# Optimization experiments

Measured on AMD Instinct MI355X. Metric: run time of the kernel, lower is better.

Reference implementation:

```python
import jax, jax.numpy as jnp
import numpy as np

N, E, IN_DIM, HID, HEADS, NUM_GRAPHS = 50000, 400000, 128, 64, 4, 256
WIDTH = HID * HEADS  # 256
NEG_SLOPE = 0.2


def setup_inputs() -> dict:
    key = jax.random.key(0)
    ks = jax.random.split(key, 20)
    inp = {
        'x': jax.random.normal(ks[0], (N, IN_DIM), dtype=jnp.float32),
        'edge_index': jax.random.randint(ks[1], (2, E), 0, N, dtype=jnp.int64),
        'edge_attr': jax.random.normal(ks[2], (E, 4), dtype=jnp.float32),
        'batch': jnp.sort(jax.random.randint(ks[3], (N,), 0, NUM_GRAPHS, dtype=jnp.int64)),
    }
    kidx = 4
    for l, in_ch in enumerate([IN_DIM, WIDTH, WIDTH]):
        s = 1.0 / np.sqrt(in_ch)
        inp[f'W{l}'] = jax.random.normal(ks[kidx], (in_ch, WIDTH), dtype=jnp.float32) * s
        inp[f'a_src{l}'] = jax.random.normal(ks[kidx + 1], (HEADS, HID), dtype=jnp.float32) * 0.1
        inp[f'a_dst{l}'] = jax.random.normal(ks[kidx + 2], (HEADS, HID), dtype=jnp.float32) * 0.1
        inp[f'b{l}'] = jnp.zeros((WIDTH,), dtype=jnp.float32)
        kidx += 3
    inp['lin_w'] = jax.random.normal(ks[kidx], (WIDTH, 1), dtype=jnp.float32) * (1.0 / np.sqrt(WIDTH))
    inp['lin_b'] = jnp.zeros((1,), dtype=jnp.float32)
    return inp


def gat_layer(x, src, dst, W, a_src, a_dst, b):
    n = x.shape[0]
    h = (x @ W).reshape(n, HEADS, HID)                      # [N,H,C]
    al_s = jnp.einsum('nhc,hc->nh', h, a_src)               # [N,H]
    al_d = jnp.einsum('nhc,hc->nh', h, a_dst)
    e = jax.nn.leaky_relu(al_s[src] + al_d[dst], NEG_SLOPE)  # [E,H]
    # segment softmax over destination node (every node has a self-loop)
    m = jax.ops.segment_max(e, dst, num_segments=n)
    e = jnp.exp(e - m[dst])
    denom = jax.ops.segment_sum(e, dst, num_segments=n)
    alpha = e / (denom[dst] + 1e-16)                         # [E,H]
    msg = h[src] * alpha[:, :, None]                         # [E,H,C]
    out = jax.ops.segment_sum(msg, dst, num_segments=n)
    return out.reshape(n, WIDTH) + b


def reference(x, edge_index, edge_attr, batch,
              W0, a_src0, a_dst0, b0,
              W1, a_src1, a_dst1, b1,
              W2, a_src2, a_dst2, b2,
              lin_w, lin_b):
    # PyG GATConv adds self-loops by default
    loops = jnp.arange(N, dtype=edge_index.dtype)
    src = jnp.concatenate([edge_index[0], loops])
    dst = jnp.concatenate([edge_index[1], loops])
    h = x
    for (W, a_s, a_d, b) in [(W0, a_src0, a_dst0, b0),
                             (W1, a_src1, a_dst1, b1),
                             (W2, a_src2, a_dst2, b2)]:
        h = jax.nn.elu(gat_layer(h, src, dst, W, a_s, a_d, b))
    pooled = jax.ops.segment_sum(h, batch, num_segments=NUM_GRAPHS)  # [G,256]
    out = pooled @ lin_w + lin_b                                     # [G,1]
    return out.squeeze(-1)
```

## Files before the change

### kernel.cpp

```cpp
#include <hip/hip_runtime.h>
#include <hip/hip_bf16.h>

#define N_NODES 50000
#define N_EDGES 400000
#define IN_DIM_ 128
#define WIDTH_ 256
#define HEADS_ 4
#define HID_ 64
#define NUM_GRAPHS_ 256
#define NEG_SLOPE_ 0.2f
#define HROW 50048

using s16x8 = __attribute__((ext_vector_type(8))) short;
using f32x4 = __attribute__((ext_vector_type(4))) float;

__device__ inline void split1(float x, short& h, short& l) {
    unsigned int u = __float_as_uint(x);
    h = (short)(u >> 16);
    float hf = __uint_as_float(u & 0xffff0000u);
    float r = x - hf;
    l = (short)(__float_as_uint(r) >> 16);
}
__device__ inline float join1(short h, short l) {
    return __uint_as_float(((unsigned int)(unsigned short)h) << 16) +
           __uint_as_float(((unsigned int)(unsigned short)l) << 16);
}

__global__ void hist_kernel(const int* __restrict__ dst, int* __restrict__ deg) {
    int e = blockIdx.x * blockDim.x + threadIdx.x;
    if (e < N_EDGES) atomicAdd(&deg[dst[e]], 1);
}

__global__ void scan1_kernel(const int* __restrict__ deg, int* __restrict__ rowptr,
                             int* __restrict__ partials) {
    __shared__ int s[256];
    int t = threadIdx.x;
    int gid = blockIdx.x * 256 + t;
    int v = (gid < N_NODES) ? deg[gid] : 0;
    s[t] = v;
    __syncthreads();
    for (int off = 1; off < 256; off <<= 1) {
        int x = 0;
        if (t >= off) x = s[t - off];
        __syncthreads();
        if (t >= off) s[t] += x;
        __syncthreads();
    }
    if (gid < N_NODES) rowptr[gid] = s[t] - v;
    if (t == 255) partials[blockIdx.x] = s[255];
}

__global__ void scan2_kernel(int* __restrict__ partials, int nb) {
    __shared__ int s[256];
    int t = threadIdx.x;
    int v = (t < nb) ? partials[t] : 0;
    s[t] = v;
    __syncthreads();
    for (int off = 1; off < 256; off <<= 1) {
        int x = 0;
        if (t >= off) x = s[t - off];
        __syncthreads();
        if (t >= off) s[t] += x;
        __syncthreads();
    }
    if (t < nb) partials[t] = s[t] - v;
}

__global__ void scan3_kernel(int* __restrict__ rowptr, const int* __restrict__ partials) {
    int gid = blockIdx.x * 256 + threadIdx.x;
    if (gid < N_NODES) rowptr[gid] += partials[blockIdx.x];
    if (gid == 0) rowptr[N_NODES] = N_EDGES;
}

__global__ void scatter_kernel(const int* __restrict__ src, const int* __restrict__ dst,
                               const int* __restrict__ rowptr, int* __restrict__ cursor,
                               int* __restrict__ csr_src) {
    int e = blockIdx.x * blockDim.x + threadIdx.x;
    if (e < N_EDGES) {
        int d = dst[e];
        int pos = rowptr[d] + atomicAdd(&cursor[d], 1);
        csr_src[pos] = src[e];
    }
}

template <int K>
__global__ void split4_kernel(const float* __restrict__ in, short* __restrict__ hi,
                              short* __restrict__ lo) {
    int idx = blockIdx.x * blockDim.x + threadIdx.x;
    if (idx >= HROW * K / 4) return;
    int e0 = idx << 2;
    int row = e0 / K;
    float4 v = make_float4(0.f, 0.f, 0.f, 0.f);
    if (row < N_NODES) v = *(const float4*)&in[e0];
    short4 h, l;
    split1(v.x, h.x, l.x);
    split1(v.y, h.y, l.y);
    split1(v.z, h.z, l.z);
    split1(v.w, h.w, l.w);
    *(short4*)&hi[e0] = h;
    *(short4*)&lo[e0] = l;
}

__global__ void wsplit_kernel(const float* __restrict__ W, short* __restrict__ Whi,
                              short* __restrict__ Wlo, int K) {
    int idx = blockIdx.x * blockDim.x + threadIdx.x;
    if (idx >= K * 256) return;
    int k = idx >> 8, n = idx & 255;
    short h, l;
    split1(W[idx], h, l);
    Whi[n * K + k] = h;
    Wlo[n * K + k] = l;
}

template <int K>
__global__ __launch_bounds__(256) void mfma_gemm(const short* __restrict__ Ahi,
                                                 const short* __restrict__ Alo,
                                                 const short* __restrict__ Bhi,
                                                 const short* __restrict__ Blo,
                                                 float* __restrict__ C) {
    const int tid = threadIdx.x;
    const int lane = tid & 63;
    const int wid = tid >> 6;
    const int wm = wid >> 1, wn = wid & 1;
    const int row0 = blockIdx.x * 128 + wm * 64;
    const int col0 = blockIdx.y * 128 + wn * 64;
    const int lr = lane & 15;
    const int lk = (lane >> 4) << 3;

    f32x4 acc[4][4] = {};

    for (int kk = 0; kk < K; kk += 32) {
        s16x8 ah[4], av[4], bh[4], bv[4];
#pragma unroll
        for (int r = 0; r < 4; ++r) {
            size_t ai = (size_t)(row0 + r * 16 + lr) * K + kk + lk;
            ah[r] = *(const s16x8*)&Ahi[ai];
            av[r] = *(const s16x8*)&Alo[ai];
            size_t bi = (size_t)(col0 + r * 16 + lr) * K + kk + lk;
            bh[r] = *(const s16x8*)&Bhi[bi];
            bv[r] = *(const s16x8*)&Blo[bi];
        }
#pragma unroll
        for (int i = 0; i < 4; ++i)
#pragma unroll
            for (int j = 0; j < 4; ++j) {
                acc[i][j] = __builtin_amdgcn_mfma_f32_16x16x32_bf16(ah[i], bh[j], acc[i][j], 0, 0, 0);
                acc[i][j] = __builtin_amdgcn_mfma_f32_16x16x32_bf16(ah[i], bv[j], acc[i][j], 0, 0, 0);
                acc[i][j] = __builtin_amdgcn_mfma_f32_16x16x32_bf16(av[i], bh[j], acc[i][j], 0, 0, 0);
            }
    }
    const int rb = (lane >> 4) << 2;
#pragma unroll
    for (int i = 0; i < 4; ++i)
#pragma unroll
        for (int q = 0; q < 4; ++q) {
            int r = row0 + i * 16 + rb + q;
#pragma unroll
            for (int j = 0; j < 4; ++j)
                C[(size_t)r * WIDTH_ + col0 + j * 16 + lr] = acc[i][j][q];
        }
}

__global__ void al_kernel(const float* __restrict__ hl, const float* __restrict__ a_src,
                          const float* __restrict__ a_dst, float* __restrict__ als,
                          float* __restrict__ ald) {
    int wid = (blockIdx.x * blockDim.x + threadIdx.x) >> 6;
    int lane = threadIdx.x & 63;
    if (wid >= N_NODES) return;
    const float4 hv = *(const float4*)&hl[(size_t)wid * WIDTH_ + (lane << 2)];
    int hd = lane >> 4;
    int j0 = (lane & 15) << 2;
    const float4 as = *(const float4*)&a_src[hd * HID_ + j0];
    const float4 ad = *(const float4*)&a_dst[hd * HID_ + j0];
    float ps = hv.x * as.x + hv.y * as.y + hv.z * as.z + hv.w * as.w;
    float pd = hv.x * ad.x + hv.y * ad.y + hv.z * ad.z + hv.w * ad.w;
    for (int off = 1; off < 16; off <<= 1) {
        ps += __shfl_xor(ps, off);
        pd += __shfl_xor(pd, off);
    }
    if ((lane & 15) == 0) {
        als[wid * 4 + hd] = ps;
        ald[wid * 4 + hd] = pd;
    }
}

__global__ void aggregate_kernel(const float* __restrict__ hl, const float* __restrict__ als,
                                 const float* __restrict__ ald_, const int* __restrict__ rowptr,
                                 const int* __restrict__ csr_src, const float* __restrict__ bias,
                                 short* __restrict__ ohi, short* __restrict__ olo) {
    int n = (blockIdx.x * blockDim.x + threadIdx.x) >> 6;
    int lane = threadIdx.x & 63;
    if (n >= N_NODES) return;
    int hd = lane >> 4;
    int c0 = lane << 2;

    float ad = ald_[n * 4 + hd];
    float e = als[n * 4 + hd] + ad;
    e = (e >= 0.f) ? e : NEG_SLOPE_ * e;
    float m = e;
    float denom = 1.0f;
    float4 hv = *(const float4*)&hl[(size_t)n * WIDTH_ + c0];
    float a0 = hv.x, a1 = hv.y, a2 = hv.z, a3 = hv.w;

    int rs = rowptr[n], re = rowptr[n + 1];
    for (int i = rs; i < re; ++i) {
        int s = csr_src[i];
        float es = als[s * 4 + hd] + ad;
        es = (es >= 0.f) ? es : NEG_SLOPE_ * es;
        float nm = fmaxf(m, es);
        float scale = expf(m - nm);
        float p = expf(es - nm);
        float4 hs = *(const float4*)&hl[(size_t)s * WIDTH_ + c0];
        a0 = a0 * scale + p * hs.x;
        a1 = a1 * scale + p * hs.y;
        a2 = a2 * scale + p * hs.z;
        a3 = a3 * scale + p * hs.w;
        denom = denom * scale + p;
        m = nm;
    }
    float inv = 1.0f / (denom + 1e-16f);
    float r0 = a0 * inv + bias[c0 + 0];
    float r1 = a1 * inv + bias[c0 + 1];
    float r2 = a2 * inv + bias[c0 + 2];
    float r3 = a3 * inv + bias[c0 + 3];
    r0 = (r0 > 0.f) ? r0 : (expf(r0) - 1.f);
    r1 = (r1 > 0.f) ? r1 : (expf(r1) - 1.f);
    r2 = (r2 > 0.f) ? r2 : (expf(r2) - 1.f);
    r3 = (r3 > 0.f) ? r3 : (expf(r3) - 1.f);
    short4 h, l;
    split1(r0, h.x, l.x);
    split1(r1, h.y, l.y);
    split1(r2, h.z, l.z);
    split1(r3, h.w, l.w);
    *(short4*)&ohi[(size_t)n * WIDTH_ + c0] = h;
    *(short4*)&olo[(size_t)n * WIDTH_ + c0] = l;
}

__global__ void out_init_kernel(const float* __restrict__ lin_b, float* __restrict__ out) {
    out[threadIdx.x] = lin_b[0];
}

__global__ void pool_kernel(const short* __restrict__ hhi, const short* __restrict__ hlo,
                            const float* __restrict__ lin_w, const int* __restrict__ batch,
                            float* __restrict__ out) {
    __shared__ float acc[NUM_GRAPHS_];
    int t = threadIdx.x;
    acc[t] = 0.f;
    __syncthreads();
    int wid = t >> 6, lane = t & 63;
    int n0 = blockIdx.x * 64;
    float4 wv = *(const float4*)&lin_w[lane << 2];
    for (int n = n0 + wid; n < n0 + 64; n += 4) {
        if (n >= N_NODES) break;
        short4 vh = *(const short4*)&hhi[(size_t)n * WIDTH_ + (lane << 2)];
        short4 vl = *(const short4*)&hlo[(size_t)n * WIDTH_ + (lane << 2)];
        float p = join1(vh.x, vl.x) * wv.x + join1(vh.y, vl.y) * wv.y +
                  join1(vh.z, vl.z) * wv.z + join1(vh.w, vl.w) * wv.w;
        for (int off = 1; off < 64; off <<= 1) p += __shfl_xor(p, off);
        if (lane == 0) atomicAdd(&acc[batch[n]], p);
    }
    __syncthreads();
    float v = acc[t];
    if (v != 0.f) atomicAdd(&out[t], v);
}

extern "C" void kernel_launch(void* const* d_in, const int* in_sizes, int n_in,
                              void* d_out, int out_size, void* d_ws, size_t ws_size,
                              hipStream_t stream) {
    const float* x = (const float*)d_in[0];
    const int* edge_index = (const int*)d_in[1];
    const int* batch = (const int*)d_in[3];
    const float* W0 = (const float*)d_in[4];
    const float* a_src0 = (const float*)d_in[5];
    const float* a_dst0 = (const float*)d_in[6];
    const float* b0 = (const float*)d_in[7];
    const float* W1 = (const float*)d_in[8];
    const float* a_src1 = (const float*)d_in[9];
    const float* a_dst1 = (const float*)d_in[10];
    const float* b1 = (const float*)d_in[11];
    const float* W2 = (const float*)d_in[12];
    const float* a_src2 = (const float*)d_in[13];
    const float* a_dst2 = (const float*)d_in[14];
    const float* b2 = (const float*)d_in[15];
    const float* lin_w = (const float*)d_in[16];
    const float* lin_b = (const float*)d_in[17];
    float* out = (float*)d_out;

    const int* e_src = edge_index;
    const int* e_dst = edge_index + N_EDGES;

    char* p = (char*)d_ws;
    float* hA = (float*)p;                p += (size_t)HROW * WIDTH_ * 4;
    short* hBhi = (short*)p;              p += (size_t)HROW * WIDTH_ * 2;
    short* hBlo = (short*)p;              p += (size_t)HROW * WIDTH_ * 2;
    short* Wt0h = (short*)p;              p += 256 * IN_DIM_ * 2;
    short* Wt0l = (short*)p;              p += 256 * IN_DIM_ * 2;
    short* Wt1h = (short*)p;              p += 256 * WIDTH_ * 2;
    short* Wt1l = (short*)p;              p += 256 * WIDTH_ * 2;
    short* Wt2h = (short*)p;              p += 256 * WIDTH_ * 2;
    short* Wt2l = (short*)p;              p += 256 * WIDTH_ * 2;
    float* als = (float*)p;               p += (size_t)HROW * 4 * 4;
    float* ald = (float*)p;               p += (size_t)HROW * 4 * 4;
    int* deg = (int*)p;                   p += HROW * 4;
    int* rowptr = (int*)p;                p += (HROW + 4) * 4;
    int* cursor = (int*)p;                p += HROW * 4;
    int* csr_src = (int*)p;               p += (size_t)N_EDGES * 4;
    int* partials = (int*)p;              p += 256 * 4;
    short* xhi = hBhi;
    short* xlo = hBhi + (size_t)HROW * IN_DIM_;

    hipMemsetAsync(deg, 0, HROW * sizeof(int), stream);
    hipMemsetAsync(cursor, 0, HROW * sizeof(int), stream);
    hist_kernel<<<(N_EDGES + 255) / 256, 256, 0, stream>>>(e_dst, deg);
    const int NB1 = (N_NODES + 255) / 256;
    scan1_kernel<<<NB1, 256, 0, stream>>>(deg, rowptr, partials);
    scan2_kernel<<<1, 256, 0, stream>>>(partials, NB1);
    scan3_kernel<<<NB1, 256, 0, stream>>>(rowptr, partials);
    scatter_kernel<<<(N_EDGES + 255) / 256, 256, 0, stream>>>(e_src, e_dst, rowptr, cursor,
                                                              csr_src);

    wsplit_kernel<<<IN_DIM_, 256, 0, stream>>>(W0, Wt0h, Wt0l, IN_DIM_);
    wsplit_kernel<<<WIDTH_, 256, 0, stream>>>(W1, Wt1h, Wt1l, WIDTH_);
    wsplit_kernel<<<WIDTH_, 256, 0, stream>>>(W2, Wt2h, Wt2l, WIDTH_);
    split4_kernel<IN_DIM_><<<(HROW * IN_DIM_ / 4 + 255) / 256, 256, 0, stream>>>(x, xhi, xlo);

    dim3 ggrid(HROW / 128, WIDTH_ / 128);
    const int NWB = (N_NODES + 3) / 4;

    mfma_gemm<IN_DIM_><<<ggrid, 256, 0, stream>>>(xhi, xlo, Wt0h, Wt0l, hA);
    al_kernel<<<NWB, 256, 0, stream>>>(hA, a_src0, a_dst0, als, ald);
    aggregate_kernel<<<NWB, 256, 0, stream>>>(hA, als, ald, rowptr, csr_src, b0, hBhi, hBlo);
    mfma_gemm<WIDTH_><<<ggrid, 256, 0, stream>>>(hBhi, hBlo, Wt1h, Wt1l, hA);
    al_kernel<<<NWB, 256, 0, stream>>>(hA, a_src1, a_dst1, als, ald);
    aggregate_kernel<<<NWB, 256, 0, stream>>>(hA, als, ald, rowptr, csr_src, b1, hBhi, hBlo);
    mfma_gemm<WIDTH_><<<ggrid, 256, 0, stream>>>(hBhi, hBlo, Wt2h, Wt2l, hA);
    al_kernel<<<NWB, 256, 0, stream>>>(hA, a_src2, a_dst2, als, ald);
    aggregate_kernel<<<NWB, 256, 0, stream>>>(hA, als, ald, rowptr, csr_src, b2, hBhi, hBlo);

    out_init_kernel<<<1, 256, 0, stream>>>(lin_b, out);
    pool_kernel<<<(N_NODES + 63) / 64, 256, 0, stream>>>(hBhi, hBlo, lin_w, batch, out);
}
```

Baseline: 602.4 us.

## Gather neighbor features in fp16 and use two-pass softmax in aggregation

The GEMM epilogue now writes an extra fp16 copy of the projected features, and the aggregation kernel gathers neighbor rows from that half-size copy instead of the fp32 buffer. The online softmax is split into two passes: a cheap max pass over the attention logits, then an accumulation pass without rescaling. expf is also replaced by the fast __expf intrinsic. This halves gather traffic and removes per-edge rescale exps, at the cost of an extra fp16 store in each GEMM, a second pass over the edge list, and fp16 rounding of the messages.

```diff
diff --git a/kernel.cpp b/kernel.cpp
--- a/kernel.cpp
+++ b/kernel.cpp
@@ -1,5 +1,6 @@
 #include <hip/hip_runtime.h>
 #include <hip/hip_bf16.h>
+#include <hip/hip_fp16.h>
 
 #define N_NODES 50000
 #define N_EDGES 400000
@@ -24,6 +25,9 @@
 __device__ inline float join1(short h, short l) {
     return __uint_as_float(((unsigned int)(unsigned short)h) << 16) +
            __uint_as_float(((unsigned int)(unsigned short)l) << 16);
+}
+__device__ inline float h2f(unsigned short u) {
+    return __half2float(__ushort_as_half(u));
 }
 
 __global__ void hist_kernel(const int* __restrict__ dst, int* __restrict__ deg) {
@@ -117,7 +121,8 @@
                                                  const short* __restrict__ Alo,
                                                  const short* __restrict__ Bhi,
                                                  const short* __restrict__ Blo,
-                                                 float* __restrict__ C) {
+                                                 float* __restrict__ C,
+                                                 __half* __restrict__ G) {
     const int tid = threadIdx.x;
     const int lane = tid & 63;
     const int wid = tid >> 6;
@@ -156,8 +161,12 @@
         for (int q = 0; q < 4; ++q) {
             int r = row0 + i * 16 + rb + q;
 #pragma unroll
-            for (int j = 0; j < 4; ++j)
-                C[(size_t)r * WIDTH_ + col0 + j * 16 + lr] = acc[i][j][q];
+            for (int j = 0; j < 4; ++j) {
+                float v = acc[i][j][q];
+                size_t idx = (size_t)r * WIDTH_ + col0 + j * 16 + lr;
+                C[idx] = v;
+                G[idx] = __float2half(v);
+            }
         }
 }
 
@@ -184,10 +193,11 @@
     }
 }
 
-__global__ void aggregate_kernel(const float* __restrict__ hl, const float* __restrict__ als,
-                                 const float* __restrict__ ald_, const int* __restrict__ rowptr,
-                                 const int* __restrict__ csr_src, const float* __restrict__ bias,
-                                 short* __restrict__ ohi, short* __restrict__ olo) {
+__global__ void aggregate_kernel(const float* __restrict__ hl, const __half* __restrict__ hg,
+                                 const float* __restrict__ als, const float* __restrict__ ald_,
+                                 const int* __restrict__ rowptr, const int* __restrict__ csr_src,
+                                 const float* __restrict__ bias, short* __restrict__ ohi,
+                                 short* __restrict__ olo) {
     int n = (blockIdx.x * blockDim.x + threadIdx.x) >> 6;
     int lane = threadIdx.x & 63;
     if (n >= N_NODES) return;
@@ -195,38 +205,42 @@
     int c0 = lane << 2;
 
     float ad = ald_[n * 4 + hd];
-    float e = als[n * 4 + hd] + ad;
-    e = (e >= 0.f) ? e : NEG_SLOPE_ * e;
-    float m = e;
-    float denom = 1.0f;
-    float4 hv = *(const float4*)&hl[(size_t)n * WIDTH_ + c0];
-    float a0 = hv.x, a1 = hv.y, a2 = hv.z, a3 = hv.w;
+    float e_self = als[n * 4 + hd] + ad;
+    e_self = (e_self >= 0.f) ? e_self : NEG_SLOPE_ * e_self;
 
     int rs = rowptr[n], re = rowptr[n + 1];
+    float m = e_self;
     for (int i = rs; i < re; ++i) {
         int s = csr_src[i];
         float es = als[s * 4 + hd] + ad;
         es = (es >= 0.f) ? es : NEG_SLOPE_ * es;
-        float nm = fmaxf(m, es);
-        float scale = expf(m - nm);
-        float p = expf(es - nm);
-        float4 hs = *(const float4*)&hl[(size_t)s * WIDTH_ + c0];
-        a0 = a0 * scale + p * hs.x;
-        a1 = a1 * scale + p * hs.y;
-        a2 = a2 * scale + p * hs.z;
-        a3 = a3 * scale + p * hs.w;
-        denom = denom * scale + p;
-        m = nm;
+        m = fmaxf(m, es);
+    }
+    float p0 = __expf(e_self - m);
+    float4 hv = *(const float4*)&hl[(size_t)n * WIDTH_ + c0];
+    float a0 = p0 * hv.x, a1 = p0 * hv.y, a2 = p0 * hv.z, a3 = p0 * hv.w;
+    float denom = p0;
+    for (int i = rs; i < re; ++i) {
+        int s = csr_src[i];
+        float es = als[s * 4 + hd] + ad;
+        es = (es >= 0.f) ? es : NEG_SLOPE_ * es;
+        float p = __expf(es - m);
+        ushort4 u = *(const ushort4*)&hg[(size_t)s * WIDTH_ + c0];
+        a0 += p * h2f(u.x);
+        a1 += p * h2f(u.y);
+        a2 += p * h2f(u.z);
+        a3 += p * h2f(u.w);
+        denom += p;
     }
     float inv = 1.0f / (denom + 1e-16f);
     float r0 = a0 * inv + bias[c0 + 0];
     float r1 = a1 * inv + bias[c0 + 1];
     float r2 = a2 * inv + bias[c0 + 2];
     float r3 = a3 * inv + bias[c0 + 3];
-    r0 = (r0 > 0.f) ? r0 : (expf(r0) - 1.f);
-    r1 = (r1 > 0.f) ? r1 : (expf(r1) - 1.f);
-    r2 = (r2 > 0.f) ? r2 : (expf(r2) - 1.f);
-    r3 = (r3 > 0.f) ? r3 : (expf(r3) - 1.f);
+    r0 = (r0 > 0.f) ? r0 : (__expf(r0) - 1.f);
+    r1 = (r1 > 0.f) ? r1 : (__expf(r1) - 1.f);
+    r2 = (r2 > 0.f) ? r2 : (__expf(r2) - 1.f);
+    r3 = (r3 > 0.f) ? r3 : (__expf(r3) - 1.f);
     short4 h, l;
     split1(r0, h.x, l.x);
     split1(r1, h.y, l.y);
@@ -291,6 +305,7 @@
 
     char* p = (char*)d_ws;
     float* hA = (float*)p;                p += (size_t)HROW * WIDTH_ * 4;
+    __half* hG = (__half*)p;              p += (size_t)HROW * WIDTH_ * 2;
     short* hBhi = (short*)p;              p += (size_t)HROW * WIDTH_ * 2;
     short* hBlo = (short*)p;              p += (size_t)HROW * WIDTH_ * 2;
     short* Wt0h = (short*)p;              p += 256 * IN_DIM_ * 2;
@@ -327,15 +342,15 @@
     dim3 ggrid(HROW / 128, WIDTH_ / 128);
     const int NWB = (N_NODES + 3) / 4;
 
-    mfma_gemm<IN_DIM_><<<ggrid, 256, 0, stream>>>(xhi, xlo, Wt0h, Wt0l, hA);
+    mfma_gemm<IN_DIM_><<<ggrid, 256, 0, stream>>>(xhi, xlo, Wt0h, Wt0l, hA, hG);
     al_kernel<<<NWB, 256, 0, stream>>>(hA, a_src0, a_dst0, als, ald);
-    aggregate_kernel<<<NWB, 256, 0, stream>>>(hA, als, ald, rowptr, csr_src, b0, hBhi, hBlo);
-    mfma_gemm<WIDTH_><<<ggrid, 256, 0, stream>>>(hBhi, hBlo, Wt1h, Wt1l, hA);
+    aggregate_kernel<<<NWB, 256, 0, stream>>>(hA, hG, als, ald, rowptr, csr_src, b0, hBhi, hBlo);
+    mfma_gemm<WIDTH_><<<ggrid, 256, 0, stream>>>(hBhi, hBlo, Wt1h, Wt1l, hA, hG);
     al_kernel<<<NWB, 256, 0, stream>>>(hA, a_src1, a_dst1, als, ald);
-    aggregate_kernel<<<NWB, 256, 0, stream>>>(hA, als, ald, rowptr, csr_src, b1, hBhi, hBlo);
-    mfma_gemm<WIDTH_><<<ggrid, 256, 0, stream>>>(hBhi, hBlo, Wt2h, Wt2l, hA);
+    aggregate_kernel<<<NWB, 256, 0, stream>>>(hA, hG, als, ald, rowptr, csr_src, b1, hBhi, hBlo);
+    mfma_gemm<WIDTH_><<<ggrid, 256, 0, stream>>>(hBhi, hBlo, Wt2h, Wt2l, hA, hG);
     al_kernel<<<NWB, 256, 0, stream>>>(hA, a_src2, a_dst2, als, ald);
-    aggregate_kernel<<<NWB, 256, 0, stream>>>(hA, als, ald, rowptr, csr_src, b2, hBhi, hBlo);
+    aggregate_kernel<<<NWB, 256, 0, stream>>>(hA, hG, als, ald, rowptr, csr_src, b2, hBhi, hBlo);
 
     out_init_kernel<<<1, 256, 0, stream>>>(lin_b, out);
     pool_kernel<<<(N_NODES + 63) / 64, 256, 0, stream>>>(hBhi, hBlo, lin_w, batch, out);
```

Result: slower. 634.5 us (+5.3%).
